# Kernel tuning notes

Hardware: AMD Instinct MI355X
Metric: run time of the kernel (lower is better)

## Reference

```python
import jax, jax.numpy as jnp
import numpy as np

B, L, D = 4, 2048, 1024
NUM_HEADS = 1
HEAD_DIM = D // NUM_HEADS  # 1024


def setup_inputs() -> dict:
    key = jax.random.key(0)
    ks = jax.random.split(key, 12)
    s = 1.0 / np.sqrt(D)
    return {
        "query": jax.random.normal(ks[0], (B, L, D), jnp.float32),
        "key": jax.random.normal(ks[1], (B, L, D), jnp.float32),
        "value": jax.random.normal(ks[2], (B, L, D), jnp.float32),
        "mask": jax.random.randint(ks[3], (B, 1, L, L), 0, 2, jnp.int32),
        "Wq": jax.random.uniform(ks[4], (D, D * NUM_HEADS), jnp.float32, -s, s),
        "bq": jnp.zeros((D * NUM_HEADS,), jnp.float32),
        "Wk": jax.random.uniform(ks[5], (D, D * NUM_HEADS), jnp.float32, -s, s),
        "bk": jnp.zeros((D * NUM_HEADS,), jnp.float32),
        "Wv": jax.random.uniform(ks[6], (D, D * NUM_HEADS), jnp.float32, -s, s),
        "bv": jnp.zeros((D * NUM_HEADS,), jnp.float32),
        "Wo": jax.random.uniform(ks[7], (D * NUM_HEADS, D), jnp.float32, -s, s),
        "bo": jnp.zeros((D,), jnp.float32),
    }


def reference(query, key, value, mask, Wq, bq, Wk, bk, Wv, bv, Wo, bo):
    b, lq = query.shape[0], query.shape[1]
    lk = key.shape[1]
    # project and split heads: (B, L, H, Dh) -> (B, H, L, Dh)
    Q = (query @ Wq + bq).reshape(b, lq, NUM_HEADS, HEAD_DIM).transpose(0, 2, 1, 3)
    K = (key @ Wk + bk).reshape(b, lk, NUM_HEADS, HEAD_DIM).transpose(0, 2, 1, 3)
    V = (value @ Wv + bv).reshape(b, lk, NUM_HEADS, HEAD_DIM).transpose(0, 2, 1, 3)
    scale = 1.0 / jnp.sqrt(jnp.float32(HEAD_DIM))
    scores = jnp.einsum("bhqd,bhkd->bhqk", Q, K) * scale  # (B,H,Lq,Lk)
    scores = jnp.where(mask == 0, jnp.float32(-1e20), scores)
    attn = jax.nn.softmax(scores, axis=-1)
    out = jnp.einsum("bhqk,bhkd->bhqd", attn, V)  # (B,H,Lq,Dh)
    out = out.transpose(0, 2, 1, 3).reshape(b, lq, NUM_HEADS * HEAD_DIM)
    return out @ Wo + bo
```

## Files before the change

kernel.cpp:

```cpp
#include <hip/hip_runtime.h>

#define B_ 4
#define L_ 2048
#define D_ 1024
#define M_FLAT (B_*L_)
#define NE_ ((size_t)M_FLAT * D_)
#define WE_ ((size_t)D_ * D_)

typedef unsigned short bf16_t;
typedef __attribute__((ext_vector_type(8))) short bf16x8;
typedef __attribute__((ext_vector_type(4))) float f32x4;

__device__ __forceinline__ bf16_t f2bf(float f) {
  union { float f; unsigned int u; } c; c.f = f;
  unsigned int u = c.u;
  unsigned int r = (u + 0x7fffu + ((u >> 16) & 1u)) >> 16;
  return (bf16_t)r;
}
__device__ __forceinline__ float bf2f(bf16_t h) {
  union { unsigned int u; float f; } c; c.u = ((unsigned int)h) << 16;
  return c.f;
}

__device__ __forceinline__ void gload_lds16(const bf16_t* g, bf16_t* l) {
  __builtin_amdgcn_global_load_lds(
      (const __attribute__((address_space(1))) unsigned int*)g,
      (__attribute__((address_space(3))) unsigned int*)l, 16, 0, 0);
}

#define BARRIER() do { asm volatile("" ::: "memory"); \
                       __builtin_amdgcn_s_barrier();  \
                       asm volatile("" ::: "memory"); } while (0)

__global__ __launch_bounds__(256) void prep_cvt(const float* __restrict__ q,
                                                const float* __restrict__ k,
                                                const float* __restrict__ v,
                                                bf16_t* __restrict__ xq) {
  const float* in; bf16_t* out; size_t li;
  int b = blockIdx.x;
  if (b < 4096)       { in = q;  out = xq;            li = (size_t)b * 256 + threadIdx.x; }
  else if (b < 8192)  { in = k;  out = xq + NE_;      li = (size_t)(b - 4096) * 256 + threadIdx.x; }
  else                { in = v;  out = xq + 2 * NE_;  li = (size_t)(b - 8192) * 256 + threadIdx.x; }
  const float4* p = (const float4*)in + li * 2;
  float4 a = p[0], bb = p[1];
  union { bf16_t h[8]; uint4 u; } r;
  r.h[0] = f2bf(a.x); r.h[1] = f2bf(a.y); r.h[2] = f2bf(a.z); r.h[3] = f2bf(a.w);
  r.h[4] = f2bf(bb.x); r.h[5] = f2bf(bb.y); r.h[6] = f2bf(bb.z); r.h[7] = f2bf(bb.w);
  ((uint4*)out)[li] = r.u;
}

__global__ __launch_bounds__(256) void transpose_cvt4(const float* __restrict__ Wq,
                                                      const float* __restrict__ Wk,
                                                      const float* __restrict__ Wo,
                                                      const float* __restrict__ Wv,
                                                      bf16_t* __restrict__ outbase) {
  __shared__ float t[32][33];
  int zz = blockIdx.z;
  int c0 = blockIdx.x * 32, r0 = blockIdx.y * 32;
  int tx = threadIdx.x, ty = threadIdx.y;
  if (zz == 3) {
    bf16_t* o = outbase + 4 * WE_;
#pragma unroll
    for (int i = 0; i < 4; i++) {
      size_t idx = (size_t)(r0 + ty + i * 8) * D_ + c0 + tx;
      o[idx] = f2bf(Wv[idx]);
    }
    return;
  }
  const float* Wsrc = (zz == 0) ? Wq : (zz == 1) ? Wk : Wo;
  bf16_t* Wt = outbase + (size_t)(zz == 2 ? 3 : zz) * WE_;
#pragma unroll
  for (int i = 0; i < 4; i++)
    t[ty + i * 8][tx] = Wsrc[(size_t)(r0 + ty + i * 8) * D_ + c0 + tx];
  __syncthreads();
#pragma unroll
  for (int i = 0; i < 4; i++)
    Wt[(size_t)(c0 + ty + i * 8) * D_ + r0 + tx] = f2bf(t[tx][ty + i * 8]);
}

__global__ __launch_bounds__(256) void c2_kernel(const float* __restrict__ bv,
                                                 const float* __restrict__ Wo,
                                                 float* __restrict__ c2) {
  int j = blockIdx.x * 256 + threadIdx.x;
  float s = 0.f;
  for (int k = 0; k < D_; k++) s += bv[k] * Wo[(size_t)k * D_ + j];
  c2[j] = s;
}

__global__ __launch_bounds__(256) void pack_mask(const int* __restrict__ mask,
                                                 unsigned long long* __restrict__ bm) {
  size_t gid = (size_t)blockIdx.x * 256 + threadIdx.x;
  int mi = mask[gid];
  unsigned long long b = __ballot(mi != 0);
  if ((threadIdx.x & 63) == 0) bm[gid >> 6] = b;
}

__global__ __launch_bounds__(256) void reduce_rsum(const float* __restrict__ rsp,
                                                   float* __restrict__ rs) {
  int r = blockIdx.x * 256 + threadIdx.x;
  float s = 0.f;
#pragma unroll
  for (int j = 0; j < 32; j++) s += rsp[(size_t)r * 32 + j];
  rs[r] = fmaxf(s, 1e-30f);
}

__global__ __launch_bounds__(256) void w2_reduce(const float* __restrict__ pw,
                                                 bf16_t* __restrict__ w2t) {
  __shared__ float t[32][33];
  int c0 = blockIdx.x * 32, r0 = blockIdx.y * 32;
  int tx = threadIdx.x, ty = threadIdx.y;
#pragma unroll
  for (int i = 0; i < 4; i++) {
    size_t idx = (size_t)(r0 + ty + i * 8) * D_ + c0 + tx;
    float s = 0.f;
#pragma unroll
    for (int zz = 0; zz < 8; zz++) s += pw[(size_t)zz * WE_ + idx];
    t[ty + i * 8][tx] = s;
  }
  __syncthreads();
#pragma unroll
  for (int i = 0; i < 4; i++)
    w2t[(size_t)(c0 + ty + i * 8) * D_ + r0 + tx] = f2bf(t[tx][ty + i * 8]);
}

#define MODE_PROJ 0
#define MODE_S    1
#define MODE_FIN  2
#define MODE_TRK  3

template <int BM, int MODE>
__global__ __launch_bounds__(512, 2)
void g8(const bf16_t* __restrict__ Abase, int lda, long strA,
        const bf16_t* __restrict__ Bbase, int ldb, long strB,
        void* __restrict__ outp, long strO, int ldo,
        const float* __restrict__ x0, const float* __restrict__ x1,
        const float* __restrict__ x2,
        const void* __restrict__ auxp, float* __restrict__ rsp,
        int K) {
  constexpr int WROWS = BM / 2;
  constexpr int QAF   = WROWS / 32;
  constexpr int MFR   = WROWS / 16;
  constexpr int AL    = BM / 128;
  constexpr int BL    = 2;
  constexpr int AHB   = WROWS * 128;
  constexpr int BUFB  = (BM + 256) * 128;
  extern __shared__ __align__(16) char smem[];

  const int tid = threadIdx.x, lane = tid & 63, w = tid >> 6;
  const int wm = w >> 2, wn = w & 3;
  const int fr = lane & 15, fs = lane >> 4;
  const int z = blockIdx.z;

  int gx = gridDim.x, nxy = gx * gridDim.y;
  int lin = blockIdx.y * gx + blockIdx.x;
  if ((nxy & 7) == 0) { int q = nxy >> 3; lin = (lin & 7) * q + (lin >> 3); }
  const int xb = lin % gx;
  const int mbase = (lin / gx) * BM, nbase = xb * 256;

  const bf16_t* A  = Abase + (size_t)z * strA;
  const bf16_t* Bt = Bbase + (size_t)z * strB;

  int offA[2][2], offB[2][2];
#pragma unroll
  for (int h = 0; h < 2; h++)
#pragma unroll
    for (int i = 0; i < 2; i++) {
      int c = i * 512 + tid, row = c >> 3;
      int sg = (c & 7) ^ (row & 7);
      if (i < AL) offA[h][i] = (mbase + h * WROWS + row) * lda + sg * 8;
      offB[h][i] = (nbase + h * 128 + row) * ldb + sg * 8;
    }

  const int swz0 = (fs ^ (fr & 7)) * 16;
  const int swz1 = ((4 + fs) ^ (fr & 7)) * 16;

  bf16x8 af[QAF][2], bfv[2][2][2];
  f32x4 acc[MFR][4] = {};

#define STAGE_A(h, kt, bsel) do {                                             \
    char* hb_ = smem + (bsel) * BUFB + (h) * AHB;                             \
    _Pragma("unroll")                                                         \
    for (int i_ = 0; i_ < AL; ++i_)                                           \
      gload_lds16(A + offA[h][i_] + (kt) * 64,                                \
                  (bf16_t*)(hb_ + (i_ * 512 + tid) * 16));                    \
  } while (0)
#define STAGE_B(h, kt, bsel) do {                                             \
    char* hb_ = smem + (bsel) * BUFB + BM * 128 + (h) * 16384;                \
    _Pragma("unroll")                                                         \
    for (int i_ = 0; i_ < BL; ++i_)                                           \
      gload_lds16(Bt + offB[h][i_] + (kt) * 64,                               \
                  (bf16_t*)(hb_ + (i_ * 512 + tid) * 16));                    \
  } while (0)
#define LOAD_A(bsel, mh) do {                                                 \
    const char* ab_ = smem + (bsel) * BUFB + (wm * WROWS) * 128;              \
    _Pragma("unroll")                                                         \
    for (int i_ = 0; i_ < QAF; ++i_) {                                        \
      int rb_ = ((mh) * (WROWS / 2) + i_ * 16 + fr) * 128;                    \
      af[i_][0] = *(const bf16x8*)(ab_ + rb_ + swz0);                         \
      af[i_][1] = *(const bf16x8*)(ab_ + rb_ + swz1);                         \
    }                                                                         \
  } while (0)
#define LOAD_B(bsel, nh) do {                                                 \
    const char* bb_ = smem + (bsel) * BUFB + BM * 128 + (wn * 64) * 128;      \
    _Pragma("unroll")                                                         \
    for (int j_ = 0; j_ < 2; ++j_) {                                          \
      int rb_ = ((nh) * 32 + j_ * 16 + fr) * 128;                             \
      bfv[nh][j_][0] = *(const bf16x8*)(bb_ + rb_ + swz0);                    \
      bfv[nh][j_][1] = *(const bf16x8*)(bb_ + rb_ + swz1);                    \
    }                                                                         \
  } while (0)
#define MFMA_Q(mh, nh) do {                                                   \
    __builtin_amdgcn_s_setprio(1);                                            \
    _Pragma("unroll")                                                         \
    for (int i_ = 0; i_ < QAF; ++i_)                                          \
    _Pragma("unroll")                                                         \
    for (int j_ = 0; j_ < 2; ++j_) {                                          \
      acc[(mh)*QAF + i_][(nh)*2 + j_] = __builtin_amdgcn_mfma_f32_16x16x32_bf16( \
          af[i_][0], bfv[nh][j_][0], acc[(mh)*QAF + i_][(nh)*2 + j_], 0, 0, 0);  \
      acc[(mh)*QAF + i_][(nh)*2 + j_] = __builtin_amdgcn_mfma_f32_16x16x32_bf16( \
          af[i_][1], bfv[nh][j_][1], acc[(mh)*QAF + i_][(nh)*2 + j_], 0, 0, 0);  \
    }                                                                         \
    __builtin_amdgcn_s_setprio(0);                                            \
  } while (0)
#define VMWN() do {                                                           \
    if constexpr (AL == 2) asm volatile("s_waitcnt vmcnt(8)" ::: "memory");   \
    else                   asm volatile("s_waitcnt vmcnt(6)" ::: "memory");   \
  } while (0)
#define LGKM0() asm volatile("s_waitcnt lgkmcnt(0)" ::: "memory")

  const int NK = K >> 6, NI = NK >> 1;

  STAGE_B(0, 0, 0); STAGE_B(1, 0, 0); STAGE_A(0, 0, 0); STAGE_A(1, 0, 0);
  STAGE_B(0, 1, 1); STAGE_B(1, 1, 1); STAGE_A(0, 1, 1); STAGE_A(1, 1, 1);
  VMWN(); BARRIER();

  for (int it = 0; it < NI; ++it) {
    const int ta = (2 * it + 2 < NK) ? 2 * it + 2 : NK - 1;
    const int tb = (2 * it + 3 < NK) ? 2 * it + 3 : NK - 1;
    LOAD_A(0, 0); LOAD_B(0, 0); MFMA_Q(0, 0);
    LOAD_B(0, 1);               MFMA_Q(0, 1);
    LOAD_A(0, 1);               MFMA_Q(1, 1);
                                MFMA_Q(1, 0);
    BARRIER();
    STAGE_B(0, ta, 0); STAGE_B(1, ta, 0); STAGE_A(0, ta, 0); STAGE_A(1, ta, 0);
    VMWN();
    BARRIER();
    LOAD_A(1, 0); LOAD_B(1, 0); MFMA_Q(0, 0);
    LOAD_B(1, 1);               MFMA_Q(0, 1);
    LOAD_A(1, 1);               MFMA_Q(1, 1);
                                MFMA_Q(1, 0);
    BARRIER();
    STAGE_B(0, tb, 1); STAGE_B(1, tb, 1); STAGE_A(0, tb, 1); STAGE_A(1, tb, 1);
    VMWN();
    BARRIER();
  }
  asm volatile("s_waitcnt vmcnt(0)" ::: "memory");

  const int r0 = mbase + wm * WROWS;
  const int c0 = nbase + wn * 64;

  if constexpr (MODE == MODE_PROJ) {
    BARRIER();
    char* ep = smem + w * AHB;
    if (z < 2) {
      bf16_t* o = (bf16_t*)outp + (size_t)z * strO;
      const float* bias = (z == 0) ? x0 : x1;
      const float scale = (z == 0) ? 0.03125f : 1.0f;
#pragma unroll
      for (int nf = 0; nf < 4; ++nf) {
        float bv = bias[c0 + nf * 16 + fr];
#pragma unroll
        for (int mf = 0; mf < MFR; ++mf)
#pragma unroll
          for (int jj = 0; jj < 4; ++jj) {
            int row = mf * 16 + fs * 4 + jj;
            int slot = (nf * 2 + (fr >> 3)) ^ ((row >> 1) & 7);
            *(bf16_t*)(ep + row * 128 + slot * 16 + (fr & 7) * 2) =
                f2bf((acc[mf][nf][jj] + bv) * scale);
          }
      }
      LGKM0();
      const int rl = lane >> 3, sl = lane & 7;
#pragma unroll
      for (int i = 0; i < WROWS / 8; ++i) {
        int row = i * 8 + rl;
        int slot = sl ^ ((row >> 1) & 7);
        uint4 vv = *(const uint4*)(ep + row * 128 + slot * 16);
        *(uint4*)&o[(size_t)(r0 + row) * ldo + c0 + sl * 8] = vv;
      }
    } else {
      bf16_t* ob = (bf16_t*)auxp;
      const int bidx = r0 >> 11, rb = r0 & (L_ - 1);
      ob += (size_t)bidx * D_ * L_;
#pragma unroll
      for (int nf = 0; nf < 4; ++nf) {
        int coll = nf * 16 + fr;
        float bv = x2[c0 + coll];
        int xm = (coll & (WROWS / 8 - 1)) << 3;
#pragma unroll
        for (int mf = 0; mf < MFR; ++mf) {
          int rbase = mf * 16 + fs * 4;
          union { bf16_t h[4]; uint2 u; } pk;
#pragma unroll
          for (int jj = 0; jj < 4; ++jj) pk.h[jj] = f2bf(acc[mf][nf][jj] + bv);
          *(uint2*)(ep + coll * (WROWS * 2) + 2 * (rbase ^ xm)) = pk.u;
        }
      }
      LGKM0();
      constexpr int LPC = WROWS / 8;
      constexpr int CPI = 64 / LPC;
      const int colr = lane / LPC;
      const int rc = (lane % LPC) * 8;
#pragma unroll
      for (int i2 = 0; i2 < LPC; ++i2) {
        int coll = i2 * CPI + colr;
        int xm = (coll & (WROWS / 8 - 1)) << 3;
        uint4 vv = *(const uint4*)(ep + coll * (WROWS * 2) + 2 * (rc ^ xm));
        *(uint4*)&ob[(size_t)(c0 + coll) * L_ + rb + rc] = vv;
      }
    }
  } else if constexpr (MODE == MODE_TRK) {
    float* o = (float*)outp + (size_t)z * strO;
#pragma unroll
    for (int mf = 0; mf < MFR; ++mf) {
#pragma unroll
      for (int jj = 0; jj < 4; ++jj) {
        int r = r0 + mf * 16 + fs * 4 + jj;
#pragma unroll
        for (int nf = 0; nf < 4; ++nf)
          o[(size_t)r * ldo + c0 + nf * 16 + fr] = acc[mf][nf][jj];
      }
    }
  } else if constexpr (MODE == MODE_S) {
    BARRIER();
    char* ep = smem + w * AHB;
    bf16_t* o = (bf16_t*)outp + (size_t)z * strO;
    const unsigned long long* bw =
        (const unsigned long long*)auxp +
        ((size_t)z * L_ + r0) * 32 + (c0 >> 6);
#pragma unroll
    for (int mf = 0; mf < MFR; ++mf) {
#pragma unroll
      for (int jj = 0; jj < 4; ++jj) {
        int row = mf * 16 + fs * 4 + jj;
        unsigned long long wd = bw[(size_t)row * 32];
        float psum = 0.f;
#pragma unroll
        for (int nf = 0; nf < 4; ++nf) {
          int cbit = nf * 16 + fr;
          float e = ((wd >> cbit) & 1ull) ? __expf(acc[mf][nf][jj]) : 0.0f;
          bf16_t eb = f2bf(e);
          psum += bf2f(eb);
          int slot = (nf * 2 + (fr >> 3)) ^ ((row >> 1) & 7);
          *(bf16_t*)(ep + row * 128 + slot * 16 + (fr & 7) * 2) = eb;
        }
#pragma unroll
        for (int off = 8; off; off >>= 1) psum += __shfl_xor(psum, off, 16);
        if (fr == 0)
          rsp[((size_t)z * L_ + r0 + row) * 32 + xb * 4 + wn] = psum;
      }
    }
    LGKM0();
    const int rl = lane >> 3, sl = lane & 7;
#pragma unroll
    for (int i = 0; i < WROWS / 8; ++i) {
      int row = i * 8 + rl;
      int slot = sl ^ ((row >> 1) & 7);
      uint4 vv = *(const uint4*)(ep + row * 128 + slot * 16);
      *(uint4*)&o[(size_t)(r0 + row) * ldo + c0 + sl * 8] = vv;
    }
  } else {
    float* o = (float*)outp + (size_t)z * strO;
    const float* rs = x0 + (size_t)z * L_;
#pragma unroll
    for (int mf = 0; mf < MFR; ++mf) {
#pragma unroll
      for (int jj = 0; jj < 4; ++jj) {
        int r = r0 + mf * 16 + fs * 4 + jj;
        float inv = 1.0f / rs[r];
#pragma unroll
        for (int nf = 0; nf < 4; ++nf) {
          int c = c0 + nf * 16 + fr;
          o[(size_t)r * ldo + c] = acc[mf][nf][jj] * inv + x1[c];
        }
      }
    }
  }
#undef STAGE_A
#undef STAGE_B
#undef LOAD_A
#undef LOAD_B
#undef MFMA_Q
#undef VMWN
#undef LGKM0
}

extern "C" void kernel_launch(void* const* d_in, const int* in_sizes, int n_in,
                              void* d_out, int out_size, void* d_ws, size_t ws_size,
                              hipStream_t stream) {
  const float* query = (const float*)d_in[0];
  const float* keyi  = (const float*)d_in[1];
  const float* value = (const float*)d_in[2];
  const int*   mask  = (const int*)d_in[3];
  const float* Wq = (const float*)d_in[4];
  const float* bq = (const float*)d_in[5];
  const float* Wk = (const float*)d_in[6];
  const float* bk = (const float*)d_in[7];
  const float* Wv = (const float*)d_in[8];
  const float* bv = (const float*)d_in[9];
  const float* Wo = (const float*)d_in[10];
  const float* bo = (const float*)d_in[11];

  bf16_t* ws = (bf16_t*)d_ws;
  bf16_t* XQ   = ws;
  bf16_t* XK   = ws + NE_;
  bf16_t* XV   = ws + 2 * NE_;
  bf16_t* WQT  = ws + 3 * NE_;
  bf16_t* WKT  = WQT + WE_;
  bf16_t* W2T  = WKT + WE_;
  bf16_t* WOT  = W2T + WE_;
  bf16_t* WVb  = WOT + WE_;
  bf16_t* Qb   = WVb + WE_;
  bf16_t* Kb   = Qb + NE_;
  bf16_t* VWt  = Kb + NE_;
  float*  rsump= (float*)(VWt + NE_);
  float*  c2p  = rsump + (size_t)B_ * L_;
  float*  rspart = c2p + D_;
  unsigned long long* bmask =
      (unsigned long long*)(rspart + (size_t)B_ * L_ * 32);
  bf16_t* Sb   = ws;
  float*  pW2  = (float*)Qb;

  hipFuncSetAttribute((const void*)g8<128, MODE_PROJ>,
                      hipFuncAttributeMaxDynamicSharedMemorySize, 98304);
  hipFuncSetAttribute((const void*)g8<256, MODE_S>,
                      hipFuncAttributeMaxDynamicSharedMemorySize, 131072);
  hipFuncSetAttribute((const void*)g8<128, MODE_TRK>,
                      hipFuncAttributeMaxDynamicSharedMemorySize, 98304);
  hipFuncSetAttribute((const void*)g8<128, MODE_FIN>,
                      hipFuncAttributeMaxDynamicSharedMemorySize, 98304);

  prep_cvt<<<dim3(12288), dim3(256), 0, stream>>>(query, keyi, value, XQ);
  pack_mask<<<dim3(65536), dim3(256), 0, stream>>>(mask, bmask);
  transpose_cvt4<<<dim3(32, 32, 4), dim3(32, 8), 0, stream>>>(Wq, Wk, Wo, Wv, WQT);
  c2_kernel<<<dim3(4), dim3(256), 0, stream>>>(bv, Wo, c2p);
  g8<128, MODE_TRK><<<dim3(4, 8, 8), 512, 98304, stream>>>(
      WVb, D_, 128, WOT, D_, 128, pW2, (long)WE_, D_,
      nullptr, nullptr, nullptr, nullptr, nullptr, 128);
  w2_reduce<<<dim3(32, 32), dim3(32, 8), 0, stream>>>(pW2, W2T);
  g8<128, MODE_PROJ><<<dim3(4, 64, 3), 512, 98304, stream>>>(
      XQ, D_, (long)NE_, WQT, D_, (long)WE_, Qb, (long)NE_, D_,
      bq, bk, c2p, VWt, nullptr, D_);
  g8<256, MODE_S><<<dim3(8, 8, 4), 512, 131072, stream>>>(
      Qb, D_, (long)L_ * D_, Kb, D_, (long)L_ * D_, Sb, (long)L_ * L_, L_,
      nullptr, nullptr, nullptr, bmask, rspart, D_);
  reduce_rsum<<<dim3(32), dim3(256), 0, stream>>>(rspart, rsump);
  g8<128, MODE_FIN><<<dim3(4, 16, 4), 512, 98304, stream>>>(
      Sb, L_, (long)L_ * L_, VWt, L_, (long)D_ * L_, d_out, (long)L_ * D_, D_,
      rsump, bo, nullptr, nullptr, nullptr, L_);
}
```

Baseline: 267.2 us.

## Merge prep kernels into one launch and fold row-sum reduction into final GEMM

Combines the four preprocessing kernels (input bf16 conversion, mask bit-packing, weight transpose/convert, bias-times-Wo vector) into a single flat-grid launch dispatched by block index. It also drops the separate row-sum reduction kernel: the final GEMM now sums the per-row partials into extra shared memory in its prologue and normalises from there. This removes several launches and inter-kernel gaps, at the cost of slightly more LDS per FIN block and a mixed-workload prep grid whose slow c2 blocks run at the tail.

```diff
diff --git a/kernel.cpp b/kernel.cpp
--- a/kernel.cpp
+++ b/kernel.cpp
@@ -32,76 +32,64 @@
                        __builtin_amdgcn_s_barrier();  \
                        asm volatile("" ::: "memory"); } while (0)
 
-__global__ __launch_bounds__(256) void prep_cvt(const float* __restrict__ q,
-                                                const float* __restrict__ k,
-                                                const float* __restrict__ v,
-                                                bf16_t* __restrict__ xq) {
-  const float* in; bf16_t* out; size_t li;
-  int b = blockIdx.x;
-  if (b < 4096)       { in = q;  out = xq;            li = (size_t)b * 256 + threadIdx.x; }
-  else if (b < 8192)  { in = k;  out = xq + NE_;      li = (size_t)(b - 4096) * 256 + threadIdx.x; }
-  else                { in = v;  out = xq + 2 * NE_;  li = (size_t)(b - 8192) * 256 + threadIdx.x; }
-  const float4* p = (const float4*)in + li * 2;
-  float4 a = p[0], bb = p[1];
-  union { bf16_t h[8]; uint4 u; } r;
-  r.h[0] = f2bf(a.x); r.h[1] = f2bf(a.y); r.h[2] = f2bf(a.z); r.h[3] = f2bf(a.w);
-  r.h[4] = f2bf(bb.x); r.h[5] = f2bf(bb.y); r.h[6] = f2bf(bb.z); r.h[7] = f2bf(bb.w);
-  ((uint4*)out)[li] = r.u;
-}
-
-__global__ __launch_bounds__(256) void transpose_cvt4(const float* __restrict__ Wq,
-                                                      const float* __restrict__ Wk,
-                                                      const float* __restrict__ Wo,
-                                                      const float* __restrict__ Wv,
-                                                      bf16_t* __restrict__ outbase) {
+__global__ __launch_bounds__(256) void prep_all(
+    const float* __restrict__ q, const float* __restrict__ k,
+    const float* __restrict__ v, const int* __restrict__ mask,
+    const float* __restrict__ Wq, const float* __restrict__ Wk,
+    const float* __restrict__ Wo, const float* __restrict__ Wv,
+    const float* __restrict__ bv,
+    bf16_t* __restrict__ outbase,
+    bf16_t* __restrict__ xq,
+    unsigned long long* __restrict__ bm,
+    float* __restrict__ c2) {
   __shared__ float t[32][33];
-  int zz = blockIdx.z;
-  int c0 = blockIdx.x * 32, r0 = blockIdx.y * 32;
-  int tx = threadIdx.x, ty = threadIdx.y;
-  if (zz == 3) {
-    bf16_t* o = outbase + 4 * WE_;
-#pragma unroll
-    for (int i = 0; i < 4; i++) {
-      size_t idx = (size_t)(r0 + ty + i * 8) * D_ + c0 + tx;
-      o[idx] = f2bf(Wv[idx]);
-    }
-    return;
+  const int b = blockIdx.x, tid = threadIdx.x;
+  if (b < 12288) {
+    const float* in; bf16_t* out; size_t li;
+    if (b < 4096)      { in = q; out = xq;           li = (size_t)b * 256 + tid; }
+    else if (b < 8192) { in = k; out = xq + NE_;     li = (size_t)(b - 4096) * 256 + tid; }
+    else               { in = v; out = xq + 2 * NE_; li = (size_t)(b - 8192) * 256 + tid; }
+    const float4* p = (const float4*)in + li * 2;
+    float4 a = p[0], bb = p[1];
+    union { bf16_t h[8]; uint4 u; } r;
+    r.h[0] = f2bf(a.x); r.h[1] = f2bf(a.y); r.h[2] = f2bf(a.z); r.h[3] = f2bf(a.w);
+    r.h[4] = f2bf(bb.x); r.h[5] = f2bf(bb.y); r.h[6] = f2bf(bb.z); r.h[7] = f2bf(bb.w);
+    ((uint4*)out)[li] = r.u;
+  } else if (b < 77824) {
+    size_t gid = (size_t)(b - 12288) * 256 + tid;
+    int mi = mask[gid];
+    unsigned long long bb = __ballot(mi != 0);
+    if ((tid & 63) == 0) bm[gid >> 6] = bb;
+  } else if (b < 81920) {
+    int bb = b - 77824;
+    int zz = bb >> 10, rem = bb & 1023;
+    int bx = rem & 31, by = rem >> 5;
+    int tx = tid & 31, ty = tid >> 5;
+    int c0 = bx * 32, r0 = by * 32;
+    if (zz == 3) {
+      bf16_t* o = outbase + 4 * WE_;
+#pragma unroll
+      for (int i = 0; i < 4; i++) {
+        size_t idx = (size_t)(r0 + ty + i * 8) * D_ + c0 + tx;
+        o[idx] = f2bf(Wv[idx]);
+      }
+      return;
+    }
+    const float* Wsrc = (zz == 0) ? Wq : (zz == 1) ? Wk : Wo;
+    bf16_t* Wt = outbase + (size_t)(zz == 2 ? 3 : zz) * WE_;
+#pragma unroll
+    for (int i = 0; i < 4; i++)
+      t[ty + i * 8][tx] = Wsrc[(size_t)(r0 + ty + i * 8) * D_ + c0 + tx];
+    __syncthreads();
+#pragma unroll
+    for (int i = 0; i < 4; i++)
+      Wt[(size_t)(c0 + ty + i * 8) * D_ + r0 + tx] = f2bf(t[tx][ty + i * 8]);
+  } else {
+    int j = (b - 81920) * 256 + tid;
+    float s = 0.f;
+    for (int kk = 0; kk < D_; kk++) s += bv[kk] * Wo[(size_t)kk * D_ + j];
+    c2[j] = s;
   }
-  const float* Wsrc = (zz == 0) ? Wq : (zz == 1) ? Wk : Wo;
-  bf16_t* Wt = outbase + (size_t)(zz == 2 ? 3 : zz) * WE_;
-#pragma unroll
-  for (int i = 0; i < 4; i++)
-    t[ty + i * 8][tx] = Wsrc[(size_t)(r0 + ty + i * 8) * D_ + c0 + tx];
-  __syncthreads();
-#pragma unroll
-  for (int i = 0; i < 4; i++)
-    Wt[(size_t)(c0 + ty + i * 8) * D_ + r0 + tx] = f2bf(t[tx][ty + i * 8]);
-}
-
-__global__ __launch_bounds__(256) void c2_kernel(const float* __restrict__ bv,
-                                                 const float* __restrict__ Wo,
-                                                 float* __restrict__ c2) {
-  int j = blockIdx.x * 256 + threadIdx.x;
-  float s = 0.f;
-  for (int k = 0; k < D_; k++) s += bv[k] * Wo[(size_t)k * D_ + j];
-  c2[j] = s;
-}
-
-__global__ __launch_bounds__(256) void pack_mask(const int* __restrict__ mask,
-                                                 unsigned long long* __restrict__ bm) {
-  size_t gid = (size_t)blockIdx.x * 256 + threadIdx.x;
-  int mi = mask[gid];
-  unsigned long long b = __ballot(mi != 0);
-  if ((threadIdx.x & 63) == 0) bm[gid >> 6] = b;
-}
-
-__global__ __launch_bounds__(256) void reduce_rsum(const float* __restrict__ rsp,
-                                                   float* __restrict__ rs) {
-  int r = blockIdx.x * 256 + threadIdx.x;
-  float s = 0.f;
-#pragma unroll
-  for (int j = 0; j < 32; j++) s += rsp[(size_t)r * 32 + j];
-  rs[r] = fmaxf(s, 1e-30f);
 }
 
 __global__ __launch_bounds__(256) void w2_reduce(const float* __restrict__ pw,
@@ -230,6 +218,17 @@
 
   const int NK = K >> 6, NI = NK >> 1;
 
+  if constexpr (MODE == MODE_FIN) {
+    float* rl = (float*)(smem + 2 * BUFB);
+    int rrow = tid >> 2, rq = tid & 3;
+    const float* rp = x0 + ((size_t)z * L_ + mbase + rrow) * 32 + rq * 8;
+    float s_ = 0.f;
+#pragma unroll
+    for (int j_ = 0; j_ < 8; ++j_) s_ += rp[j_];
+    rl[rrow * 4 + rq] = s_;
+    LGKM0();
+  }
+
   STAGE_B(0, 0, 0); STAGE_B(1, 0, 0); STAGE_A(0, 0, 0); STAGE_A(1, 0, 0);
   STAGE_B(0, 1, 1); STAGE_B(1, 1, 1); STAGE_A(0, 1, 1); STAGE_A(1, 1, 1);
   VMWN(); BARRIER();
@@ -371,13 +370,16 @@
     }
   } else {
     float* o = (float*)outp + (size_t)z * strO;
-    const float* rs = x0 + (size_t)z * L_;
+    const float* rl = (const float*)(smem + 2 * BUFB);
 #pragma unroll
     for (int mf = 0; mf < MFR; ++mf) {
 #pragma unroll
       for (int jj = 0; jj < 4; ++jj) {
         int r = r0 + mf * 16 + fs * 4 + jj;
-        float inv = 1.0f / rs[r];
+        int rloc = wm * WROWS + mf * 16 + fs * 4 + jj;
+        float rsv = rl[rloc * 4] + rl[rloc * 4 + 1] +
+                    rl[rloc * 4 + 2] + rl[rloc * 4 + 3];
+        float inv = 1.0f / fmaxf(rsv, 1e-30f);
 #pragma unroll
         for (int nf = 0; nf < 4; ++nf) {
           int c = c0 + nf * 16 + fr;
@@ -423,8 +425,7 @@
   bf16_t* Qb   = WVb + WE_;
   bf16_t* Kb   = Qb + NE_;
   bf16_t* VWt  = Kb + NE_;
-  float*  rsump= (float*)(VWt + NE_);
-  float*  c2p  = rsump + (size_t)B_ * L_;
+  float*  c2p  = (float*)(VWt + NE_);
   float*  rspart = c2p + D_;
   unsigned long long* bmask =
       (unsigned long long*)(rspart + (size_t)B_ * L_ * 32);
@@ -438,12 +439,10 @@
   hipFuncSetAttribute((const void*)g8<128, MODE_TRK>,
                       hipFuncAttributeMaxDynamicSharedMemorySize, 98304);
   hipFuncSetAttribute((const void*)g8<128, MODE_FIN>,
-                      hipFuncAttributeMaxDynamicSharedMemorySize, 98304);
-
-  prep_cvt<<<dim3(12288), dim3(256), 0, stream>>>(query, keyi, value, XQ);
-  pack_mask<<<dim3(65536), dim3(256), 0, stream>>>(mask, bmask);
-  transpose_cvt4<<<dim3(32, 32, 4), dim3(32, 8), 0, stream>>>(Wq, Wk, Wo, Wv, WQT);
-  c2_kernel<<<dim3(4), dim3(256), 0, stream>>>(bv, Wo, c2p);
+                      hipFuncAttributeMaxDynamicSharedMemorySize, 100352);
+
+  prep_all<<<dim3(81924), dim3(256), 0, stream>>>(
+      query, keyi, value, mask, Wq, Wk, Wo, Wv, bv, WQT, XQ, bmask, c2p);
   g8<128, MODE_TRK><<<dim3(4, 8, 8), 512, 98304, stream>>>(
       WVb, D_, 128, WOT, D_, 128, pW2, (long)WE_, D_,
       nullptr, nullptr, nullptr, nullptr, nullptr, 128);
@@ -454,8 +453,7 @@
   g8<256, MODE_S><<<dim3(8, 8, 4), 512, 131072, stream>>>(
       Qb, D_, (long)L_ * D_, Kb, D_, (long)L_ * D_, Sb, (long)L_ * L_, L_,
       nullptr, nullptr, nullptr, bmask, rspart, D_);
-  reduce_rsum<<<dim3(32), dim3(256), 0, stream>>>(rspart, rsump);
-  g8<128, MODE_FIN><<<dim3(4, 16, 4), 512, 98304, stream>>>(
+  g8<128, MODE_FIN><<<dim3(4, 16, 4), 512, 100352, stream>>>(
       Sb, L_, (long)L_ * L_, VWt, L_, (long)D_ * L_, d_out, (long)L_ * D_, D_,
-      rsump, bo, nullptr, nullptr, nullptr, L_);
-}
+      rspart, bo, nullptr, nullptr, nullptr, L_);
+}
```

After: 258.8 us. 1.03x faster.
